# Optimization experiments

Measured on AMD Instinct MI355X. Metric: run time of the kernel, lower is better.

The kernel has to match this reference:

```python
import jax, jax.numpy as jnp
import numpy as np

N, E, G = 50000, 800000, 64
L, C, IN, H, OUT = 3, 4, 64, 64, 64
BN_EPS = 1e-5


def setup_inputs() -> dict:
    key = jax.random.key(0)
    ks = jax.random.split(key, 12)
    x = jax.random.normal(ks[0], (N, IN), dtype=jnp.float32)
    cluster_labels = jax.random.randint(ks[1], (N,), 0, C, dtype=jnp.int32)
    edge_index = jax.random.randint(ks[2], (2, E), 0, N, dtype=jnp.int64)
    batch = jnp.sort(jax.random.randint(ks[3], (N,), 0, G, dtype=jnp.int64))
    s1 = 1.0 / np.sqrt(H)
    # per (layer, cluster) GIN MLP params: Lin(H,H) -> BN -> ReLU -> Lin(H,H)
    W1 = jax.random.normal(ks[4], (L, C, H, H), dtype=jnp.float32) * s1
    b1 = jnp.zeros((L, C, H), dtype=jnp.float32)
    g1 = jnp.ones((L, C, H), dtype=jnp.float32)
    be1 = jnp.zeros((L, C, H), dtype=jnp.float32)
    W2 = jax.random.normal(ks[5], (L, C, H, H), dtype=jnp.float32) * s1
    b2 = jnp.zeros((L, C, H), dtype=jnp.float32)
    # pool MLP: Lin(H*L, H) -> BN -> ReLU -> Lin(H, OUT)
    Wp1 = jax.random.normal(ks[6], (H * L, H), dtype=jnp.float32) / np.sqrt(H * L)
    bp1 = jnp.zeros((H,), dtype=jnp.float32)
    gp = jnp.ones((H,), dtype=jnp.float32)
    bep = jnp.zeros((H,), dtype=jnp.float32)
    Wp2 = jax.random.normal(ks[7], (H, OUT), dtype=jnp.float32) * s1
    bp2 = jnp.zeros((OUT,), dtype=jnp.float32)
    return {"x": x, "cluster_labels": cluster_labels, "edge_index": edge_index,
            "batch": batch, "W1": W1, "b1": b1, "g1": g1, "be1": be1,
            "W2": W2, "b2": b2, "Wp1": Wp1, "bp1": bp1, "gp": gp,
            "bep": bep, "Wp2": Wp2, "bp2": bp2}


def _masked_bn(h, mf, gamma, beta):
    # BatchNorm computed only over rows where mask is set (those are the rows fed to nn)
    cnt = jnp.maximum(mf.sum(), 1.0)
    mean = (mf[:, None] * h).sum(0) / cnt
    var = (mf[:, None] * (h - mean) ** 2).sum(0) / cnt
    return (h - mean) * jax.lax.rsqrt(var + BN_EPS) * gamma + beta


def _bn(h, gamma, beta):
    mean = h.mean(0)
    var = ((h - mean) ** 2).mean(0)
    return (h - mean) * jax.lax.rsqrt(var + BN_EPS) * gamma + beta


def reference(x, cluster_labels, edge_index, batch, W1, b1, g1, be1, W2, b2,
              Wp1, bp1, gp, bep, Wp2, bp2):
    src, dst = edge_index[0], edge_index[1]
    pooled = []
    for t in range(L):
        for c in range(C):
            mask = cluster_labels == c
            mf = mask.astype(x.dtype)
            # GIN aggregation: out[i] = sum_{j -> i} x[j]
            agg = jax.ops.segment_sum(x[src], dst, num_segments=N)
            h = agg + x  # (1 + eps) * x residual with eps = 0
            h = h @ W1[t, c] + b1[t, c]
            h = jax.nn.relu(_masked_bn(h, mf, g1[t, c], be1[t, c]))
            h = h @ W2[t, c] + b2[t, c]
            x = jnp.where(mask[:, None], h, x)
        pooled.append(jax.ops.segment_sum(x, batch, num_segments=G))
    z = jnp.concatenate(pooled, axis=1)  # [G, H*L]
    z = z @ Wp1 + bp1
    z = jax.nn.relu(_bn(z, gp, bep))
    return z @ Wp2 + bp2
```

## Files before the change

kernel.cpp:

```cpp
#include <hip/hip_runtime.h>
#include <hip/hip_bf16.h>

#define NN 50000
#define EE 800000
#define GG 64
#define LL 3
#define CC 4
#define HH 64
#define BN_EPS 1e-5f
#define NSHADOW 4
#define SBLK 196
#define GIN_BLOCKS 2048
#define MM_BLOCKS 256


typedef __attribute__((ext_vector_type(8))) short bf16x8;
typedef __attribute__((ext_vector_type(4))) float f32x4;

__device__ __forceinline__ float bf2f(short s) {
    return __int_as_float(((int)(unsigned short)s) << 16);
}
__device__ __forceinline__ short f2bf(float v) {
    __hip_bfloat16 hb = __float2bfloat16(v);
    return *(short*)&hb;
}


__global__ void k_deghist(const int* __restrict__ dst, int* __restrict__ deg,
                          const int* __restrict__ labels, int* __restrict__ blockcnt,
                          const float* __restrict__ x_in, __hip_bfloat16* __restrict__ xw) {
    __shared__ int cnt[CC];
    int tid = threadIdx.x;
    for (int i = blockIdx.x * 256 + tid; i < NN * 64; i += gridDim.x * 256)
        xw[i] = __float2bfloat16(x_in[i]);
    bool hist = (blockIdx.x < SBLK);
    if (hist && tid < CC) cnt[tid] = 0;
    __syncthreads();
    int gid = blockIdx.x * 256 + tid;
    if (gid < EE) atomicAdd(&deg[dst[gid]], 1);
    if (hist && gid < NN) atomicAdd(&cnt[labels[gid]], 1);
    __syncthreads();
    if (hist && tid < CC) blockcnt[tid * SBLK + blockIdx.x] = cnt[tid];
}

__global__ void k_wpack(const float* __restrict__ W1, const float* __restrict__ W2,
                        short* __restrict__ wf) {
    int o = blockIdx.x * 256 + threadIdx.x;
    if (o >= 24 * 4096) return;
    int m = o >> 12;
    int r = o & 4095;
    int colt = r >> 10;
    int fragk = (r >> 9) & 1;
    int lane = (r >> 3) & 63;
    int j = r & 7;
    int k = fragk * 32 + ((lane >> 4) << 3) + j;
    int n = colt * 16 + (lane & 15);
    const float* src = (m < 12) ? (W1 + (size_t)m * 4096) : (W2 + (size_t)(m - 12) * 4096);
    wf[o] = f2bf(src[k * 64 + n]);
}

__global__ __launch_bounds__(256) void k_scancombo(
    const int* __restrict__ deg, int* __restrict__ rowptr, int* __restrict__ dpart,
    const int* __restrict__ blockcnt, int* __restrict__ coffs, int* __restrict__ ccount) {
    __shared__ int smem[CC * 256];
    int tid = threadIdx.x;
    if (blockIdx.x < SBLK) {
        int i = blockIdx.x * 256 + tid;
        int v = (i < NN) ? deg[i] : 0;
        smem[tid] = v;
        __syncthreads();
        for (int off = 1; off < 256; off <<= 1) {
            int u = (tid >= off) ? smem[tid - off] : 0;
            __syncthreads();
            smem[tid] += u;
            __syncthreads();
        }
        if (i < NN) rowptr[i] = smem[tid] - v;
        if (tid == 255) dpart[blockIdx.x] = smem[255];
    } else {
        int own[CC];
        for (int c = 0; c < CC; c++) {
            own[c] = (tid < SBLK) ? blockcnt[c * SBLK + tid] : 0;
            smem[c * 256 + tid] = own[c];
        }
        __syncthreads();
        for (int off = 1; off < 256; off <<= 1) {
            int v[CC];
            for (int c = 0; c < CC; c++) v[c] = (tid >= off) ? smem[c * 256 + tid - off] : 0;
            __syncthreads();
            for (int c = 0; c < CC; c++) smem[c * 256 + tid] += v[c];
            __syncthreads();
        }
        if (tid < SBLK)
            for (int c = 0; c < CC; c++) coffs[c * SBLK + tid] = smem[c * 256 + tid] - own[c];
        if (tid == 0)
            for (int c = 0; c < CC; c++) ccount[c] = smem[c * 256 + 255];
    }
}

__global__ __launch_bounds__(256) void k_dscan2(int* __restrict__ dpart,
                                                int* __restrict__ dbase,
                                                int* __restrict__ rowptr) {
    __shared__ int s[256];
    int tid = threadIdx.x;
    int v = (tid < SBLK) ? dpart[tid] : 0;
    s[tid] = v;
    __syncthreads();
    for (int off = 1; off < 256; off <<= 1) {
        int u = (tid >= off) ? s[tid - off] : 0;
        __syncthreads();
        s[tid] += u;
        __syncthreads();
    }
    if (tid < SBLK) dbase[tid] = s[tid] - v;
    if (tid == 0) rowptr[NN] = EE;
}

__global__ __launch_bounds__(256) void k_cfill_dscan3(
    int* __restrict__ rowptr, const int* __restrict__ dbase, int* __restrict__ cursor,
    const int* __restrict__ labels, const int* __restrict__ coffs, int* __restrict__ clist) {
    __shared__ int pos[CC];
    int tid = threadIdx.x;
    if (tid < CC) pos[tid] = coffs[tid * SBLK + blockIdx.x];
    __syncthreads();
    int i = blockIdx.x * 256 + tid;
    if (i < NN) {
        int r = rowptr[i] + dbase[blockIdx.x];
        rowptr[i] = r;
        cursor[i] = r;
        int c = labels[i];
        int p = atomicAdd(&pos[c], 1);
        clist[c * NN + p] = i;
    }
}

__global__ void k_fill(const int* __restrict__ src, const int* __restrict__ dst,
                       int* __restrict__ cursor, int* __restrict__ adj) {
    int e = blockIdx.x * blockDim.x + threadIdx.x;
    if (e < EE) {
        int d = dst[e];
        int pos = atomicAdd(&cursor[d], 1);
        adj[pos] = src[e] << 7;
    }
}

__global__ __launch_bounds__(256) void k_gather(
    const __hip_bfloat16* __restrict__ xw, const int* __restrict__ adj,
    const int* __restrict__ rowptr, const int* __restrict__ clist_c,
    const int* __restrict__ ccount_c, __hip_bfloat16* __restrict__ aggbuf,
    const int* __restrict__ batch, float* __restrict__ z, int tpool) {
    int cnt = *ccount_c;
    int lane = threadIdx.x & 63;
    int wave = threadIdx.x >> 6;
    int wid = blockIdx.x * 4 + wave;
    int nwaves = gridDim.x * 4;
    const char* xwb = (const char*)xw;
    int idx = wid;
    int node_next = (idx < cnt) ? clist_c[idx] : 0;
    for (; idx < cnt; idx += nwaves) {
        int node = node_next;
        int nidx = idx + nwaves;
        if (nidx < cnt) node_next = clist_c[nidx];
        int rb = rowptr[node], re = rowptr[node + 1];
        float a0 = __bfloat162float(xw[(size_t)node * 64 + lane]);
        float a1 = 0.f, a2 = 0.f, a3 = 0.f, a4 = 0.f, a5 = 0.f, a6 = 0.f, a7 = 0.f;
        int base = rb, rem = re - rb;
        while (rem > 0) {
            int take = min(rem, 64);
            int nb = adj[base + min(lane, take - 1)];
            int j = 0;
            for (; j + 8 <= take; j += 8) {
                int o0 = __builtin_amdgcn_readlane(nb, j + 0);
                int o1 = __builtin_amdgcn_readlane(nb, j + 1);
                int o2 = __builtin_amdgcn_readlane(nb, j + 2);
                int o3 = __builtin_amdgcn_readlane(nb, j + 3);
                int o4 = __builtin_amdgcn_readlane(nb, j + 4);
                int o5 = __builtin_amdgcn_readlane(nb, j + 5);
                int o6 = __builtin_amdgcn_readlane(nb, j + 6);
                int o7 = __builtin_amdgcn_readlane(nb, j + 7);
                a0 += __bfloat162float(((const __hip_bfloat16*)(xwb + o0))[lane]);
                a1 += __bfloat162float(((const __hip_bfloat16*)(xwb + o1))[lane]);
                a2 += __bfloat162float(((const __hip_bfloat16*)(xwb + o2))[lane]);
                a3 += __bfloat162float(((const __hip_bfloat16*)(xwb + o3))[lane]);
                a4 += __bfloat162float(((const __hip_bfloat16*)(xwb + o4))[lane]);
                a5 += __bfloat162float(((const __hip_bfloat16*)(xwb + o5))[lane]);
                a6 += __bfloat162float(((const __hip_bfloat16*)(xwb + o6))[lane]);
                a7 += __bfloat162float(((const __hip_bfloat16*)(xwb + o7))[lane]);
            }
            for (; j < take; j++) {
                int o = __builtin_amdgcn_readlane(nb, j);
                a0 += __bfloat162float(((const __hip_bfloat16*)(xwb + o))[lane]);
            }
            base += take; rem -= take;
        }
        float acc = ((a0 + a1) + (a2 + a3)) + ((a4 + a5) + (a6 + a7));
        aggbuf[(size_t)idx * 64 + lane] = __float2bfloat16(acc);
    }
    if (tpool >= 0) {
        int lo = wid * 64;
        if (lo < NN) {
            int hi = min(lo + 64, NN);
            float acc = 0.f;
            int curg = batch[lo];
            for (int n = lo; n < hi; n++) {
                int g = batch[n];
                if (g != curg) {
                    atomicAdd(&z[curg * (HH * LL) + tpool * HH + lane], acc);
                    acc = 0.f;
                    curg = g;
                }
                acc += __bfloat162float(xw[(size_t)n * 64 + lane]);
            }
            atomicAdd(&z[curg * (HH * LL) + tpool * HH + lane], acc);
        }
    }
}

__global__ __launch_bounds__(256) void k_lin1(
    const __hip_bfloat16* __restrict__ aggbuf, const int* __restrict__ ccount_c,
    const short* __restrict__ wf1, const float* __restrict__ b1c,
    __hip_bfloat16* __restrict__ h1buf, float* __restrict__ bnacc) {
    int cnt = *ccount_c;
    int tiles = (cnt + 15) >> 4;
    int lane = threadIdx.x & 63;
    int wave = threadIdx.x >> 6;
    int wid = blockIdx.x * 4 + wave;
    int nwaves = gridDim.x * 4;
    int quad = lane >> 4;
    int l15 = lane & 15;

    bf16x8 wb[8];
    #pragma unroll
    for (int f = 0; f < 8; f++)
        wb[f] = *(const bf16x8*)(wf1 + f * 512 + lane * 8);
    float bcol[4];
    #pragma unroll
    for (int colt = 0; colt < 4; colt++) bcol[colt] = b1c[colt * 16 + l15];

    float sS[4] = {0.f, 0.f, 0.f, 0.f};
    float sQ[4] = {0.f, 0.f, 0.f, 0.f};

    for (int tile = wid; tile < tiles; tile += nwaves) {
        int tb = tile << 4;
        int row = tb + l15;
        const __hip_bfloat16* ar = aggbuf + (size_t)row * 64 + quad * 8;
        bf16x8 a0 = *(const bf16x8*)ar;
        bf16x8 a1 = *(const bf16x8*)(ar + 32);
        #pragma unroll
        for (int colt = 0; colt < 4; colt++) {
            f32x4 acc = {0.f, 0.f, 0.f, 0.f};
            acc = __builtin_amdgcn_mfma_f32_16x16x32_bf16(a0, wb[colt * 2 + 0], acc, 0, 0, 0);
            acc = __builtin_amdgcn_mfma_f32_16x16x32_bf16(a1, wb[colt * 2 + 1], acc, 0, 0, 0);
            #pragma unroll
            for (int r = 0; r < 4; r++) {
                int nrow = tb + quad * 4 + r;
                if (nrow < cnt) {
                    float s = acc[r] + bcol[colt];
                    __hip_bfloat16 hb = __float2bfloat16(s);
                    h1buf[(size_t)nrow * 64 + colt * 16 + l15] = hb;
                    float st = __bfloat162float(hb);
                    sS[colt] += st;
                    sQ[colt] += st * st;
                }
            }
        }
    }
    #pragma unroll
    for (int colt = 0; colt < 4; colt++) {
        sS[colt] += __shfl_xor(sS[colt], 16); sS[colt] += __shfl_xor(sS[colt], 32);
        sQ[colt] += __shfl_xor(sQ[colt], 16); sQ[colt] += __shfl_xor(sQ[colt], 32);
    }
    if (quad == 0) {
        int slot = (blockIdx.x & (NSHADOW - 1)) * 128;
        #pragma unroll
        for (int colt = 0; colt < 4; colt++) {
            atomicAdd(&bnacc[slot + colt * 16 + l15], sS[colt]);
            atomicAdd(&bnacc[slot + 64 + colt * 16 + l15], sQ[colt]);
        }
    }
}

__global__ __launch_bounds__(256) void k_cmfma(
    __hip_bfloat16* __restrict__ xw, const int* __restrict__ clist_c,
    const int* __restrict__ ccount_c, const float* __restrict__ g1c,
    const float* __restrict__ be1c, const short* __restrict__ wf2,
    const float* __restrict__ b2c, const __hip_bfloat16* __restrict__ h1buf,
    const float* __restrict__ bnacc) {
    __shared__ float lds_scale[64];
    __shared__ float lds_shift[64];
    int cnt = *ccount_c;
    int tiles = (cnt + 15) >> 4;
    int lane = threadIdx.x & 63;
    int wave = threadIdx.x >> 6;
    int wid = blockIdx.x * 4 + wave;
    int nwaves = gridDim.x * 4;
    int quad = lane >> 4;
    int l15 = lane & 15;

    if (threadIdx.x < 64) {
        float s = 0.f, q = 0.f;
        #pragma unroll
        for (int sh = 0; sh < NSHADOW; sh++) {
            s += bnacc[sh * 128 + threadIdx.x];
            q += bnacc[sh * 128 + 64 + threadIdx.x];
        }
        float fc = fmaxf((float)cnt, 1.f);
        float mean = s / fc;
        float var = q / fc - mean * mean;
        float sc = g1c[threadIdx.x] * rsqrtf(var + BN_EPS);
        lds_scale[threadIdx.x] = sc;
        lds_shift[threadIdx.x] = be1c[threadIdx.x] - mean * sc;
    }
    __syncthreads();

    bf16x8 wb[8];
    #pragma unroll
    for (int f = 0; f < 8; f++)
        wb[f] = *(const bf16x8*)(wf2 + f * 512 + lane * 8);
    float bcol[4];
    #pragma unroll
    for (int colt = 0; colt < 4; colt++) bcol[colt] = b2c[colt * 16 + l15];
    float scl0[8], sft0[8], scl1[8], sft1[8];
    #pragma unroll
    for (int j = 0; j < 8; j++) {
        int ch = quad * 8 + j;
        scl0[j] = lds_scale[ch];      sft0[j] = lds_shift[ch];
        scl1[j] = lds_scale[ch + 32]; sft1[j] = lds_shift[ch + 32];
    }

    for (int tile = wid; tile < tiles; tile += nwaves) {
        int tb = tile << 4;
        int row = tb + l15;
        const __hip_bfloat16* hr = h1buf + (size_t)row * 64 + quad * 8;
        bf16x8 h0 = *(const bf16x8*)hr;
        bf16x8 h1f = *(const bf16x8*)(hr + 32);
        bf16x8 a0, a1;
        #pragma unroll
        for (int j = 0; j < 8; j++) {
            a0[j] = f2bf(fmaxf(bf2f(h0[j]) * scl0[j] + sft0[j], 0.f));
            a1[j] = f2bf(fmaxf(bf2f(h1f[j]) * scl1[j] + sft1[j], 0.f));
        }
        #pragma unroll
        for (int colt = 0; colt < 4; colt++) {
            f32x4 acc = {0.f, 0.f, 0.f, 0.f};
            acc = __builtin_amdgcn_mfma_f32_16x16x32_bf16(a0, wb[colt * 2 + 0], acc, 0, 0, 0);
            acc = __builtin_amdgcn_mfma_f32_16x16x32_bf16(a1, wb[colt * 2 + 1], acc, 0, 0, 0);
            #pragma unroll
            for (int r = 0; r < 4; r++) {
                int nrow = tb + quad * 4 + r;
                if (nrow < cnt) {
                    int node = clist_c[nrow];
                    xw[(size_t)node * 64 + colt * 16 + l15] =
                        __float2bfloat16(acc[r] + bcol[colt]);
                }
            }
        }
    }
}

__global__ void k_pool(const __hip_bfloat16* __restrict__ xw, const int* __restrict__ batch,
                       float* __restrict__ z, int t) {
    const int CHUNK = 64;
    int lane = threadIdx.x & 63;
    int wg = (blockIdx.x * blockDim.x + threadIdx.x) >> 6;
    int lo = wg * CHUNK;
    if (lo >= NN) return;
    int hi = min(lo + CHUNK, NN);
    float acc = 0.f;
    int curg = batch[lo];
    for (int n = lo; n < hi; n++) {
        int g = batch[n];
        if (g != curg) {
            atomicAdd(&z[curg * (HH * LL) + t * HH + lane], acc);
            acc = 0.f;
            curg = g;
        }
        acc += __bfloat162float(xw[(size_t)n * 64 + lane]);
    }
    atomicAdd(&z[curg * (HH * LL) + t * HH + lane], acc);
}

__global__ __launch_bounds__(256) void k_final1(
    const float* __restrict__ z, const float* __restrict__ Wp1,
    const float* __restrict__ bp1, float* __restrict__ hbuf) {
    __shared__ float red[256];
    int g = blockIdx.x;
    int k = threadIdx.x & 63;
    int part = threadIdx.x >> 6;
    float s = 0.f;
    #pragma unroll 8
    for (int j = part * 48; j < (part + 1) * 48; j++)
        s += z[g * (HH * LL) + j] * Wp1[j * 64 + k];
    red[threadIdx.x] = s;
    __syncthreads();
    if (part == 0)
        hbuf[g * 64 + k] = red[k] + red[64 + k] + red[128 + k] + red[192 + k] + bp1[k];
}

__global__ __launch_bounds__(256) void k_final2(
    const float* __restrict__ hbuf, const float* __restrict__ gp,
    const float* __restrict__ bep, const float* __restrict__ Wp2,
    const float* __restrict__ bp2, float* __restrict__ out) {
    __shared__ float lds[64 * 64];
    __shared__ float sscale[64];
    __shared__ float sshift[64];
    int tid = threadIdx.x;
    for (int i = tid; i < 64 * 64; i += 256) lds[i] = hbuf[i];
    __syncthreads();
    if (tid < 64) {
        float s = 0.f, q = 0.f;
        for (int g = 0; g < 64; g++) { float v = lds[g * 64 + tid]; s += v; q += v * v; }
        float mean = s / 64.f;
        float var = q / 64.f - mean * mean;
        float sc = gp[tid] * rsqrtf(var + BN_EPS);
        sscale[tid] = sc;
        sshift[tid] = bep[tid] - mean * sc;
    }
    __syncthreads();
    for (int i = tid; i < 64 * 64; i += 256) {
        int k = i & 63;
        lds[i] = fmaxf(lds[i] * sscale[k] + sshift[k], 0.f);
    }
    __syncthreads();
    for (int i = tid; i < 64 * 64; i += 256) {
        int g = i >> 6, o = i & 63;
        float s = bp2[o];
        #pragma unroll 8
        for (int k = 0; k < 64; k++) s += lds[g * 64 + k] * Wp2[k * 64 + o];
        out[g * 64 + o] = s;
    }
}

extern "C" void kernel_launch(void* const* d_in, const int* in_sizes, int n_in,
                              void* d_out, int out_size, void* d_ws, size_t ws_size,
                              hipStream_t stream) {
    const float* x_in = (const float*)d_in[0];
    const int* labels = (const int*)d_in[1];
    const int* esrc = (const int*)d_in[2];
    const int* edst = esrc + EE;
    const int* batch = (const int*)d_in[3];
    const float* W1 = (const float*)d_in[4];
    const float* b1 = (const float*)d_in[5];
    const float* g1 = (const float*)d_in[6];
    const float* be1 = (const float*)d_in[7];
    const float* W2 = (const float*)d_in[8];
    const float* b2 = (const float*)d_in[9];
    const float* Wp1 = (const float*)d_in[10];
    const float* bp1 = (const float*)d_in[11];
    const float* gp = (const float*)d_in[12];
    const float* bep = (const float*)d_in[13];
    const float* Wp2 = (const float*)d_in[14];
    const float* bp2 = (const float*)d_in[15];
    float* out = (float*)d_out;

    char* p = (char*)d_ws;
    auto carve = [&](size_t bytes) -> void* {
        void* r = (void*)p;
        p += (bytes + 255) & ~(size_t)255;
        return r;
    };
    float* bnacc = (float*)carve((size_t)LL * CC * NSHADOW * 128 * 4);
    float* z     = (float*)carve((size_t)GG * HH * LL * 4);
    int*   deg   = (int*)carve((size_t)NN * 4);
    size_t zero_bytes = (size_t)(p - (char*)d_ws);
    int*   ccount  = (int*)carve(CC * 4);
    int*   blockcnt= (int*)carve((size_t)CC * SBLK * 4);
    int*   coffs   = (int*)carve((size_t)CC * SBLK * 4);
    int*   dpart   = (int*)carve((size_t)SBLK * 4);
    int*   dbase   = (int*)carve((size_t)SBLK * 4);
    __hip_bfloat16* xw     = (__hip_bfloat16*)carve((size_t)NN * 64 * 2);
    __hip_bfloat16* aggbuf = (__hip_bfloat16*)carve((size_t)NN * 64 * 2);
    __hip_bfloat16* h1buf  = (__hip_bfloat16*)carve((size_t)NN * 64 * 2);
    short* wf      = (short*)carve((size_t)24 * 4096 * 2);
    float* hbuf    = (float*)carve((size_t)GG * 64 * 4);
    int*   rowptr  = (int*)carve((size_t)(NN + 1) * 4);
    int*   cursor  = (int*)carve((size_t)NN * 4);
    int*   adj     = (int*)carve((size_t)EE * 4);
    int*   clist   = (int*)carve((size_t)CC * NN * 4);

    hipMemsetAsync(d_ws, 0, zero_bytes, stream);

    k_deghist<<<(EE + 255) / 256, 256, 0, stream>>>(edst, deg, labels, blockcnt, x_in, xw);
    k_wpack<<<(24 * 4096 + 255) / 256, 256, 0, stream>>>(W1, W2, wf);
    k_scancombo<<<SBLK + 1, 256, 0, stream>>>(deg, rowptr, dpart, blockcnt, coffs, ccount);
    k_dscan2<<<1, 256, 0, stream>>>(dpart, dbase, rowptr);
    k_cfill_dscan3<<<SBLK, 256, 0, stream>>>(rowptr, dbase, cursor, labels, coffs, clist);
    k_fill<<<(EE + 255) / 256, 256, 0, stream>>>(esrc, edst, cursor, adj);

    for (int t = 0; t < LL; t++) {
        for (int c = 0; c < CC; c++) {
            int tc = t * CC + c;
            int tpool = (c == 0) ? (t - 1) : -1;
            k_gather<<<GIN_BLOCKS, 256, 0, stream>>>(
                xw, adj, rowptr, clist + c * NN, ccount + c, aggbuf, batch, z, tpool);
            k_lin1<<<MM_BLOCKS, 256, 0, stream>>>(
                aggbuf, ccount + c, wf + (size_t)tc * 4096, b1 + (size_t)tc * 64,
                h1buf, bnacc + (size_t)tc * NSHADOW * 128);
            k_cmfma<<<MM_BLOCKS, 256, 0, stream>>>(
                xw, clist + c * NN, ccount + c,
                g1 + (size_t)tc * 64, be1 + (size_t)tc * 64,
                wf + (size_t)(12 + tc) * 4096, b2 + (size_t)tc * 64,
                h1buf, bnacc + (size_t)tc * NSHADOW * 128);
        }
    }
    {
        int pool_waves = (NN + 63) / 64;
        int pool_blocks = (pool_waves * 64 + 255) / 256;
        k_pool<<<pool_blocks, 256, 0, stream>>>(xw, batch, z, LL - 1);
    }
    k_final1<<<GG, 256, 0, stream>>>(z, Wp1, bp1, hbuf);
    k_final2<<<1, 256, 0, stream>>>(hbuf, gp, bep, Wp2, bp2, out);
}
```

Measured before the change: 563.4 us.

## Fuse weight packing into deghist, range-partition CSR fill, widen gather unroll

Moves the weight-packing work into the degree-histogram kernel so one launch is dropped. The CSR fill kernel now runs 8 passes over the edge list, each handling only destinations in one node range, so atomics and adjacency writes land in a narrower address window; the cost is reading the edge list eight times. The gather loop gets a 16-way unrolled accumulator path so more neighbor loads are in flight, at the cost of more registers per lane.

```diff
diff --git a/kernel.cpp b/kernel.cpp
--- a/kernel.cpp
+++ b/kernel.cpp
@@ -12,6 +12,8 @@
 #define SBLK 196
 #define GIN_BLOCKS 2048
 #define MM_BLOCKS 256
+#define ECHUNKS 3125
+#define NODE_RANGE 6250
 
 
 typedef __attribute__((ext_vector_type(8))) short bf16x8;
@@ -28,11 +30,26 @@
 
 __global__ void k_deghist(const int* __restrict__ dst, int* __restrict__ deg,
                           const int* __restrict__ labels, int* __restrict__ blockcnt,
-                          const float* __restrict__ x_in, __hip_bfloat16* __restrict__ xw) {
+                          const float* __restrict__ x_in, __hip_bfloat16* __restrict__ xw,
+                          const float* __restrict__ W1, const float* __restrict__ W2,
+                          short* __restrict__ wf) {
     __shared__ int cnt[CC];
     int tid = threadIdx.x;
     for (int i = blockIdx.x * 256 + tid; i < NN * 64; i += gridDim.x * 256)
         xw[i] = __float2bfloat16(x_in[i]);
+    int o = blockIdx.x * 256 + tid;
+    if (o < 24 * 4096) {
+        int m = o >> 12;
+        int r = o & 4095;
+        int colt = r >> 10;
+        int fragk = (r >> 9) & 1;
+        int lane = (r >> 3) & 63;
+        int j = r & 7;
+        int k = fragk * 32 + ((lane >> 4) << 3) + j;
+        int n = colt * 16 + (lane & 15);
+        const float* src = (m < 12) ? (W1 + (size_t)m * 4096) : (W2 + (size_t)(m - 12) * 4096);
+        wf[o] = f2bf(src[k * 64 + n]);
+    }
     bool hist = (blockIdx.x < SBLK);
     if (hist && tid < CC) cnt[tid] = 0;
     __syncthreads();
@@ -41,22 +58,6 @@
     if (hist && gid < NN) atomicAdd(&cnt[labels[gid]], 1);
     __syncthreads();
     if (hist && tid < CC) blockcnt[tid * SBLK + blockIdx.x] = cnt[tid];
-}
-
-__global__ void k_wpack(const float* __restrict__ W1, const float* __restrict__ W2,
-                        short* __restrict__ wf) {
-    int o = blockIdx.x * 256 + threadIdx.x;
-    if (o >= 24 * 4096) return;
-    int m = o >> 12;
-    int r = o & 4095;
-    int colt = r >> 10;
-    int fragk = (r >> 9) & 1;
-    int lane = (r >> 3) & 63;
-    int j = r & 7;
-    int k = fragk * 32 + ((lane >> 4) << 3) + j;
-    int n = colt * 16 + (lane & 15);
-    const float* src = (m < 12) ? (W1 + (size_t)m * 4096) : (W2 + (size_t)(m - 12) * 4096);
-    wf[o] = f2bf(src[k * 64 + n]);
 }
 
 __global__ __launch_bounds__(256) void k_scancombo(
@@ -136,11 +137,15 @@
 
 __global__ void k_fill(const int* __restrict__ src, const int* __restrict__ dst,
                        int* __restrict__ cursor, int* __restrict__ adj) {
-    int e = blockIdx.x * blockDim.x + threadIdx.x;
+    int range = blockIdx.x / ECHUNKS;
+    int e = (blockIdx.x - range * ECHUNKS) * 256 + threadIdx.x;
     if (e < EE) {
         int d = dst[e];
-        int pos = atomicAdd(&cursor[d], 1);
-        adj[pos] = src[e] << 7;
+        int lo = range * NODE_RANGE;
+        if (d >= lo && d < lo + NODE_RANGE) {
+            int pos = atomicAdd(&cursor[d], 1);
+            adj[pos] = src[e] << 7;
+        }
     }
 }
 
@@ -162,38 +167,37 @@
         int nidx = idx + nwaves;
         if (nidx < cnt) node_next = clist_c[nidx];
         int rb = rowptr[node], re = rowptr[node + 1];
-        float a0 = __bfloat162float(xw[(size_t)node * 64 + lane]);
-        float a1 = 0.f, a2 = 0.f, a3 = 0.f, a4 = 0.f, a5 = 0.f, a6 = 0.f, a7 = 0.f;
+        float a[16];
+        a[0] = __bfloat162float(xw[(size_t)node * 64 + lane]);
+        #pragma unroll
+        for (int u = 1; u < 16; u++) a[u] = 0.f;
         int base = rb, rem = re - rb;
         while (rem > 0) {
             int take = min(rem, 64);
             int nb = adj[base + min(lane, take - 1)];
             int j = 0;
+            for (; j + 16 <= take; j += 16) {
+                #pragma unroll
+                for (int u = 0; u < 16; u++) {
+                    int o = __builtin_amdgcn_readlane(nb, j + u);
+                    a[u] += __bfloat162float(((const __hip_bfloat16*)(xwb + o))[lane]);
+                }
+            }
             for (; j + 8 <= take; j += 8) {
-                int o0 = __builtin_amdgcn_readlane(nb, j + 0);
-                int o1 = __builtin_amdgcn_readlane(nb, j + 1);
-                int o2 = __builtin_amdgcn_readlane(nb, j + 2);
-                int o3 = __builtin_amdgcn_readlane(nb, j + 3);
-                int o4 = __builtin_amdgcn_readlane(nb, j + 4);
-                int o5 = __builtin_amdgcn_readlane(nb, j + 5);
-                int o6 = __builtin_amdgcn_readlane(nb, j + 6);
-                int o7 = __builtin_amdgcn_readlane(nb, j + 7);
-                a0 += __bfloat162float(((const __hip_bfloat16*)(xwb + o0))[lane]);
-                a1 += __bfloat162float(((const __hip_bfloat16*)(xwb + o1))[lane]);
-                a2 += __bfloat162float(((const __hip_bfloat16*)(xwb + o2))[lane]);
-                a3 += __bfloat162float(((const __hip_bfloat16*)(xwb + o3))[lane]);
-                a4 += __bfloat162float(((const __hip_bfloat16*)(xwb + o4))[lane]);
-                a5 += __bfloat162float(((const __hip_bfloat16*)(xwb + o5))[lane]);
-                a6 += __bfloat162float(((const __hip_bfloat16*)(xwb + o6))[lane]);
-                a7 += __bfloat162float(((const __hip_bfloat16*)(xwb + o7))[lane]);
+                #pragma unroll
+                for (int u = 0; u < 8; u++) {
+                    int o = __builtin_amdgcn_readlane(nb, j + u);
+                    a[u] += __bfloat162float(((const __hip_bfloat16*)(xwb + o))[lane]);
+                }
             }
             for (; j < take; j++) {
                 int o = __builtin_amdgcn_readlane(nb, j);
-                a0 += __bfloat162float(((const __hip_bfloat16*)(xwb + o))[lane]);
+                a[0] += __bfloat162float(((const __hip_bfloat16*)(xwb + o))[lane]);
             }
             base += take; rem -= take;
         }
-        float acc = ((a0 + a1) + (a2 + a3)) + ((a4 + a5) + (a6 + a7));
+        float acc = (((a[0] + a[1]) + (a[2] + a[3])) + ((a[4] + a[5]) + (a[6] + a[7]))) +
+                    (((a[8] + a[9]) + (a[10] + a[11])) + ((a[12] + a[13]) + (a[14] + a[15])));
         aggbuf[(size_t)idx * 64 + lane] = __float2bfloat16(acc);
     }
     if (tpool >= 0) {
@@ -480,12 +484,11 @@
 
     hipMemsetAsync(d_ws, 0, zero_bytes, stream);
 
-    k_deghist<<<(EE + 255) / 256, 256, 0, stream>>>(edst, deg, labels, blockcnt, x_in, xw);
-    k_wpack<<<(24 * 4096 + 255) / 256, 256, 0, stream>>>(W1, W2, wf);
+    k_deghist<<<ECHUNKS, 256, 0, stream>>>(edst, deg, labels, blockcnt, x_in, xw, W1, W2, wf);
     k_scancombo<<<SBLK + 1, 256, 0, stream>>>(deg, rowptr, dpart, blockcnt, coffs, ccount);
     k_dscan2<<<1, 256, 0, stream>>>(dpart, dbase, rowptr);
     k_cfill_dscan3<<<SBLK, 256, 0, stream>>>(rowptr, dbase, cursor, labels, coffs, clist);
-    k_fill<<<(EE + 255) / 256, 256, 0, stream>>>(esrc, edst, cursor, adj);
+    k_fill<<<ECHUNKS * 8, 256, 0, stream>>>(esrc, edst, cursor, adj);
 
     for (int t = 0; t < LL; t++) {
         for (int c = 0; c < CC; c++) {
```

After: 555.7 us. Within noise of the previous version (-1.4%).
